# Performance work log

Measured on AMD Instinct MI355X. Metric: run time of the kernel, lower is better.

Reference implementation:

```python
import jax, jax.numpy as jnp
import numpy as np

# ---- config (matches init_kwargs) ----
L_LEVELS = 10          # int(log(8192/16)/log(2)) + 1
LEVEL_DIM = 4
BASE_RES = 16
LOG2_T = 21
BOUND = 2.0            # contract() output bound
DENSITY_BIAS = -1.0
RGB_PADDING = 0.001
DEG_VIEW = 4
PRIME1 = np.uint32(2654435761)
PRIME2 = np.uint32(805459861)


def _grid_meta():
    # torch-ngp GridEncoder layout: per-level scale = base*2^l - 1 (per_level_scale=2),
    # resolution = base*2^l, params = min(2^21, (res+1)^3) rounded up to multiple of 8.
    offsets, scales, res_list, sizes = [0], [], [], []
    for l in range(L_LEVELS):
        res = BASE_RES * (2 ** l)
        scales.append(float(res - 1))
        n = min(2 ** LOG2_T, (res + 1) ** 3)
        n = int(np.ceil(n / 8) * 8)
        res_list.append(res)
        sizes.append(n)
        offsets.append(offsets[-1] + n)
    return scales, res_list, sizes, offsets

GRID_SCALES, GRID_RES, GRID_SIZES, GRID_OFFSETS = _grid_meta()
TOTAL_PARAMS = GRID_OFFSETS[-1]  # 14995560
CORNERS = np.array([[(c >> d) & 1 for d in range(3)] for c in range(8)], dtype=np.int32)


def contract(x):
    # mipnerf360 contraction, output in [-2, 2]
    eps = jnp.finfo(x.dtype).eps
    x_mag_sq = jnp.maximum(eps, jnp.sum(x * x, axis=-1, keepdims=True))
    return jnp.where(x_mag_sq <= 1.0, x, ((2.0 * jnp.sqrt(x_mag_sq) - 1.0) / x_mag_sq) * x)


def pos_enc(x):
    # coord.pos_enc with identity, min_deg=0, max_deg=DEG_VIEW -> dim 3 + 3*2*4 = 27
    scales = 2.0 ** jnp.arange(DEG_VIEW, dtype=x.dtype)
    xb = (x[..., None, :] * scales[:, None]).reshape(x.shape[:-1] + (3 * DEG_VIEW,))
    four = jnp.sin(jnp.concatenate([xb, xb + 0.5 * jnp.pi], axis=-1))
    return jnp.concatenate([x, four], axis=-1)


def grid_encode(x01, embeddings):
    # x01: [N,3] in [0,1]; embeddings: [TOTAL_PARAMS, LEVEL_DIM]
    feats = []
    for l in range(L_LEVELS):
        pos = x01 * GRID_SCALES[l] + 0.5  # align_corners=False
        pos_floor = jnp.floor(pos)
        frac = pos - pos_floor            # trilinear weights, differentiable in x01
        pg = pos_floor.astype(jnp.int32)  # [N,3]
        res1 = GRID_RES[l] + 1
        size = GRID_SIZES[l]
        use_hash = (res1 ** 3) > size
        lvl_emb = embeddings[GRID_OFFSETS[l]:GRID_OFFSETS[l] + size]
        acc = jnp.zeros(x01.shape[:-1] + (LEVEL_DIM,), x01.dtype)
        for c in range(8):
            off = CORNERS[c]
            corner = pg + off[None, :]
            if use_hash:
                cu = corner.astype(jnp.uint32)
                idx = (cu[:, 0] ^ (cu[:, 1] * PRIME1) ^ (cu[:, 2] * PRIME2)) % jnp.uint32(size)
                idx = idx.astype(jnp.int32)
            else:
                idx = corner[:, 0] + corner[:, 1] * res1 + corner[:, 2] * (res1 * res1)
            w = jnp.prod(jnp.where(off[None, :] == 1, frac, 1.0 - frac), axis=-1)  # [N]
            acc = acc + w[:, None] * lvl_emb[idx]
        feats.append(acc)
    return jnp.concatenate(feats, axis=-1)  # [N, 40]


def setup_inputs() -> dict:
    key = jax.random.key(0)
    ks = jax.random.split(key, 10)
    R, S = 2048, 32
    coords = jax.random.normal(ks[0], (R, S, 3), jnp.float32) * 1.5
    viewdirs = jax.random.normal(ks[1], (R, 3), jnp.float32)
    viewdirs = viewdirs / jnp.linalg.norm(viewdirs, axis=-1, keepdims=True)
    embeddings = (jax.random.uniform(ks[2], (TOTAL_PARAMS, LEVEL_DIM), jnp.float32) * 2.0 - 1.0) * 1e-4

    def lin(k, fan_in, fan_out):
        k1, k2 = jax.random.split(k)
        lim = 1.0 / np.sqrt(fan_in)
        w = jax.random.uniform(k1, (fan_in, fan_out), jnp.float32, -lim, lim)
        b = jax.random.uniform(k2, (fan_out,), jnp.float32, -lim, lim)
        return w, b

    w_d1, b_d1 = lin(ks[3], L_LEVELS * LEVEL_DIM, 64)
    w_d2, b_d2 = lin(ks[4], 64, 256)
    DIR_DIM = 3 + 3 * 2 * DEG_VIEW  # 27
    w_r0, b_r0 = lin(ks[5], 256 + DIR_DIM, 256)          # 283 -> 256
    w_r1, b_r1 = lin(ks[6], 256 + 256 + DIR_DIM, 256)    # skip concat: 539 -> 256
    w_rgb, b_rgb = lin(ks[7], 256, 3)
    return dict(coords=coords, viewdirs=viewdirs, embeddings=embeddings,
                w_d1=w_d1, b_d1=b_d1, w_d2=w_d2, b_d2=b_d2,
                w_r0=w_r0, b_r0=b_r0, w_r1=w_r1, b_r1=b_r1,
                w_rgb=w_rgb, b_rgb=b_rgb)


def reference(coords, viewdirs, embeddings, w_d1, b_d1, w_d2, b_d2,
              w_r0, b_r0, w_r1, b_r1, w_rgb, b_rgb):
    shape = coords.shape[:-1]  # (rays, samples)
    cw = contract(coords) / BOUND          # coords_warped, in [-1, 1]
    x01 = (cw.reshape(-1, 3) + BOUND) / (2.0 * BOUND)  # encoder normalization with bound=2
    feats = grid_encode(x01, embeddings)               # [N, 40]
    h = jax.nn.relu(feats @ w_d1 + b_d1)
    x = h @ w_d2 + b_d2                                # [N, 256]
    raw_density = x[:, 0].reshape(shape)
    density = jax.nn.softplus(raw_density + DENSITY_BIAS)
    bottleneck = x.reshape(shape + (256,))
    dir_enc = pos_enc(viewdirs)                        # [rays, 27]
    dir_enc = jnp.broadcast_to(dir_enc[..., None, :], shape + (dir_enc.shape[-1],))
    inp = jnp.concatenate([bottleneck, dir_enc], axis=-1)  # [rays, S, 283]
    y = jax.nn.relu(inp @ w_r0 + b_r0)
    y = jnp.concatenate([y, inp], axis=-1)             # skip at layer i == skip_layer_dir == 0
    y = jax.nn.relu(y @ w_r1 + b_r1)
    rgb = jax.nn.sigmoid(y @ w_rgb + b_rgb)            # rgb_premultiplier=1, rgb_bias=0
    rgb = rgb * (1.0 + 2.0 * RGB_PADDING) - RGB_PADDING
    return cw, density, rgb
```

## Files before the change

### kernel.cpp

```cpp
#include <hip/hip_runtime.h>
#include <math.h>

#define NS 65536
#define NRAYS 2048

typedef __attribute__((ext_vector_type(8))) short short8;
typedef __attribute__((ext_vector_type(4))) float f32x4;
typedef unsigned short u16;

#define OFF_FEATS 0ull
#define OFF_HBF   10485760ull
#define OFF_DW0   85983232ull
#define OFF_DW1   88080384ull
#define OFF_WD2T  90177536ull
#define OFF_WR0T  90210304ull
#define OFF_WR1T  90341376ull

#define OUT_DENS 196608
#define OUT_RGB  262144

__device__ __forceinline__ u16 f2b(float f) {
    unsigned u = __builtin_bit_cast(unsigned, f);
    return (u16)((u + 0x7FFFu + ((u >> 16) & 1u)) >> 16);
}

__global__ __launch_bounds__(256) void cvt_weights(
    const float* __restrict__ w_d2, const float* __restrict__ w_r0,
    const float* __restrict__ w_r1, u16* __restrict__ wd2t,
    u16* __restrict__ wr0t, u16* __restrict__ wr1t)
{
    int idx = blockIdx.x * 256 + threadIdx.x;
    if (idx < 16384)  wd2t[idx] = f2b(w_d2[(idx & 63)  * 256 + (idx >> 6)]);
    if (idx < 65536)  wr0t[idx] = f2b(w_r0[(idx & 255) * 256 + (idx >> 8)]);
    if (idx < 131072) wr1t[idx] = f2b(w_r1[(idx & 511) * 256 + (idx >> 9)]);
}

__global__ __launch_bounds__(256) void dir_kernel(
    const float* __restrict__ viewdirs,
    const float* __restrict__ w_r0, const float* __restrict__ b_r0,
    const float* __restrict__ w_r1, const float* __restrict__ b_r1,
    float* __restrict__ dirW0, float* __restrict__ dirW1)
{
    __shared__ float de[27];
    int ray = blockIdx.x, t = threadIdx.x;
    if (t < 27) {
        float v;
        if (t < 3) v = viewdirs[3*ray + t];
        else {
            int k = (t - 3) % 12;
            float b = viewdirs[3*ray + (k % 3)] * (float)(1 << (k / 3));
            v = (t < 15) ? sinf(b) : sinf(b + 1.5707964f);
        }
        de[t] = v;
    }
    __syncthreads();
    float a0 = b_r0[t], a1 = b_r1[t];
#pragma unroll
    for (int d = 0; d < 27; ++d) {
        a0 = fmaf(de[d], w_r0[(256+d)*256 + t], a0);
        a1 = fmaf(de[d], w_r1[(512+d)*256 + t], a1);
    }
    dirW0[ray*256 + t] = a0;
    dirW1[ray*256 + t] = a1;
}

__global__ __launch_bounds__(256) void encode_kernel(
    const float* __restrict__ coords, const float* __restrict__ emb,
    float* __restrict__ cw_out, float* __restrict__ featsT)
{
    int t = threadIdx.x;
    int l = blockIdx.x >> 8;
    int i = ((blockIdx.x & 255) << 8) + t;
    float x = coords[3*i], y = coords[3*i+1], z = coords[3*i+2];
    float m2 = fmaxf(x*x + y*y + z*z, 1.1920928955078125e-07f);
    float cx = x, cy = y, cz = z;
    if (m2 > 1.0f) { float s = (2.0f*sqrtf(m2) - 1.0f)/m2; cx*=s; cy*=s; cz*=s; }
    cx *= 0.5f; cy *= 0.5f; cz *= 0.5f;
    if (l == 0) { cw_out[3*i]=cx; cw_out[3*i+1]=cy; cw_out[3*i+2]=cz; }
    float u0 = (cx + 2.0f)*0.25f, u1 = (cy + 2.0f)*0.25f, u2 = (cz + 2.0f)*0.25f;

    int res = 16 << l;
    int res1 = res + 1;
    float scale = (float)(res - 1);
    unsigned off = (l >= 3) ? 315496u + (unsigned)(l-3)*2097152u
                            : (l == 0 ? 0u : (l == 1 ? 4920u : 40864u));
    float p0 = u0*scale + 0.5f, p1 = u1*scale + 0.5f, p2 = u2*scale + 0.5f;
    float f0 = floorf(p0), f1 = floorf(p1), f2 = floorf(p2);
    float fr0 = p0-f0, fr1 = p1-f1, fr2 = p2-f2;
    unsigned g0 = (unsigned)(int)f0, g1 = (unsigned)(int)f1, g2 = (unsigned)(int)f2;
    float a0=0.f, a1=0.f, a2=0.f, a3=0.f;
    bool use_hash = (l >= 3);
#pragma unroll
    for (int c = 0; c < 8; ++c) {
        unsigned ox = c & 1u, oy = (c >> 1) & 1u, oz = (c >> 2) & 1u;
        unsigned qx = g0 + ox, qy = g1 + oy, qz = g2 + oz;
        unsigned idx;
        if (use_hash) idx = (qx ^ (qy*2654435761u) ^ (qz*805459861u)) & 2097151u;
        else          idx = qx + qy*(unsigned)res1 + qz*(unsigned)(res1*res1);
        const float4 e = *(const float4*)(emb + 4u*(off + idx));
        float w = (ox ? fr0 : 1.0f-fr0) * (oy ? fr1 : 1.0f-fr1) * (oz ? fr2 : 1.0f-fr2);
        a0 = fmaf(w, e.x, a0); a1 = fmaf(w, e.y, a1);
        a2 = fmaf(w, e.z, a2); a3 = fmaf(w, e.w, a3);
    }
    featsT[(4*l+0)*NS + i] = a0;
    featsT[(4*l+1)*NS + i] = a1;
    featsT[(4*l+2)*NS + i] = a2;
    featsT[(4*l+3)*NS + i] = a3;
}

__global__ __launch_bounds__(256) void gemm_d1_kernel(
    const float* __restrict__ featsT, const float* __restrict__ w_d1,
    const float* __restrict__ b_d1, const float* __restrict__ w_d2,
    const float* __restrict__ b_d2, u16* __restrict__ h_bf,
    float* __restrict__ dens)
{
    __shared__ float As[40][256];
    __shared__ float Ws[40*64];
    __shared__ float wc0[64];
    int t = threadIdx.x;
    int m0 = blockIdx.x * 256;
#pragma unroll
    for (int k = 0; k < 40; ++k) As[k][t] = featsT[k*NS + m0 + t];
#pragma unroll
    for (int i = 0; i < 10; ++i) Ws[i*256 + t] = w_d1[i*256 + t];
    if (t < 64) wc0[t] = w_d2[t*256];
    __syncthreads();
    int tn = t & 3, tm = t >> 2;
    float acc[4][16] = {};
#pragma unroll
    for (int k = 0; k < 40; ++k) {
        float4 a = *(const float4*)&As[k][tm*4];
        float av[4] = {a.x, a.y, a.z, a.w};
        const float4* wp = (const float4*)&Ws[k*64 + tn*16];
#pragma unroll
        for (int r = 0; r < 4; ++r) {
            float4 w = wp[r];
            float wv[4] = {w.x, w.y, w.z, w.w};
#pragma unroll
            for (int ii = 0; ii < 4; ++ii)
#pragma unroll
                for (int cc = 0; cc < 4; ++cc)
                    acc[ii][r*4+cc] = fmaf(av[ii], wv[cc], acc[ii][r*4+cc]);
        }
    }
    float p[4] = {0.f, 0.f, 0.f, 0.f};
#pragma unroll
    for (int jj = 0; jj < 16; ++jj) {
        int j = tn*16 + jj;
        float bj = b_d1[j], w0 = wc0[j];
#pragma unroll
        for (int ii = 0; ii < 4; ++ii) {
            float h = fmaxf(acc[ii][jj] + bj, 0.f);
            acc[ii][jj] = h;
            p[ii] = fmaf(h, w0, p[ii]);
        }
    }
#pragma unroll
    for (int ii = 0; ii < 4; ++ii) {
        int s = m0 + tm*4 + ii;
        unsigned u[8];
#pragma unroll
        for (int q = 0; q < 8; ++q)
            u[q] = (unsigned)f2b(acc[ii][2*q]) | ((unsigned)f2b(acc[ii][2*q+1]) << 16);
        uint4 v0 = {u[0], u[1], u[2], u[3]};
        uint4 v1 = {u[4], u[5], u[6], u[7]};
        *(uint4*)(h_bf + (size_t)s*64 + tn*16)     = v0;
        *(uint4*)(h_bf + (size_t)s*64 + tn*16 + 8) = v1;
    }
#pragma unroll
    for (int ii = 0; ii < 4; ++ii) {
        p[ii] += __shfl_xor(p[ii], 1, 64);
        p[ii] += __shfl_xor(p[ii], 2, 64);
    }
    if (tn == 0) {
        float b0 = b_d2[0];
#pragma unroll
        for (int ii = 0; ii < 4; ++ii) {
            float z = p[ii] + b0 - 1.0f;
            dens[m0 + tm*4 + ii] = fmaxf(z, 0.f) + log1pf(expf(-fabsf(z)));
        }
    }
}

#define MFMA __builtin_amdgcn_mfma_f32_16x16x32_bf16

__global__ __launch_bounds__(256) void mfma_tail(
    const u16* __restrict__ h_bf, const u16* __restrict__ wd2t,
    const u16* __restrict__ w0t, const u16* __restrict__ w1t,
    const float* __restrict__ b_d2, const float* __restrict__ dirW0,
    const float* __restrict__ dirW1, const float* __restrict__ w_rgb,
    const float* __restrict__ b_rgb, float* __restrict__ rgb)
{
    __shared__ u16 tileX[8192];
    __shared__ u16 tileY[8192];
    __shared__ float pp[4][32][3];
    int t = threadIdx.x, lane = t & 63, w = t >> 6;
    int m0 = blockIdx.x * 32;
    int rl = lane & 15, kg = (lane >> 4) * 8;
    int ro = (lane >> 4) * 4;
    unsigned swA = ((unsigned)(rl & 7)) << 4;
    const char* txc = (const char*)tileX;
    const char* tyc = (const char*)tileY;
    f32x4 zero = {0.f,0.f,0.f,0.f};

    f32x4 acc[2][4];

#pragma unroll
    for (int a = 0; a < 2; ++a)
#pragma unroll
        for (int b = 0; b < 4; ++b) acc[a][b] = zero;
    {
        const u16* pA0 = h_bf + (size_t)(m0 + rl)*64 + kg;
        const u16* pA1 = h_bf + (size_t)(m0 + 16 + rl)*64 + kg;
        const u16* pBd = wd2t + (w*64 + rl)*64 + kg;
#pragma unroll
        for (int ks = 0; ks < 2; ++ks) {
            int kb = ks*32;
            short8 a0 = *(const short8*)(pA0 + kb);
            short8 a1 = *(const short8*)(pA1 + kb);
#pragma unroll
            for (int nt = 0; nt < 4; ++nt) {
                short8 b = *(const short8*)(pBd + nt*1024 + kb);
                acc[0][nt] = MFMA(a0, b, acc[0][nt], 0, 0, 0);
                acc[1][nt] = MFMA(a1, b, acc[1][nt], 0, 0, 0);
            }
        }
    }
#pragma unroll
    for (int nt = 0; nt < 4; ++nt) {
        int col = w*64 + nt*16 + rl;
        float bias = b_d2[col];
#pragma unroll
        for (int mt = 0; mt < 2; ++mt)
#pragma unroll
            for (int r = 0; r < 4; ++r) {
                int row = mt*16 + ro + r;
                unsigned byte = (unsigned)(row*512 + col*2) ^ ((unsigned)(row & 7) << 4);
                tileX[byte >> 1] = f2b(acc[mt][nt][r] + bias);
            }
    }
    __syncthreads();

#pragma unroll
    for (int a = 0; a < 2; ++a)
#pragma unroll
        for (int b = 0; b < 4; ++b) acc[a][b] = zero;
    {
        const u16* pB0 = w0t + (w*64 + rl)*256 + kg;
#pragma unroll
        for (int ks = 0; ks < 8; ++ks) {
            int kb = ks*32;
            unsigned base = (unsigned)((kb + kg)*2);
            short8 a0 = *(const short8*)(txc + (((unsigned)(rl*512)      + base) ^ swA));
            short8 a1 = *(const short8*)(txc + (((unsigned)((16+rl)*512) + base) ^ swA));
#pragma unroll
            for (int nt = 0; nt < 4; ++nt) {
                short8 b = *(const short8*)(pB0 + nt*4096 + kb);
                acc[0][nt] = MFMA(a0, b, acc[0][nt], 0, 0, 0);
                acc[1][nt] = MFMA(a1, b, acc[1][nt], 0, 0, 0);
            }
        }
    }
    {
        const float* dir0 = dirW0 + (m0 >> 5)*256;
#pragma unroll
        for (int nt = 0; nt < 4; ++nt) {
            int col = w*64 + nt*16 + rl;
            float bias = dir0[col];
#pragma unroll
            for (int mt = 0; mt < 2; ++mt)
#pragma unroll
                for (int r = 0; r < 4; ++r) {
                    int row = mt*16 + ro + r;
                    unsigned byte = (unsigned)(row*512 + col*2) ^ ((unsigned)(row & 7) << 4);
                    tileY[byte >> 1] = f2b(fmaxf(acc[mt][nt][r] + bias, 0.f));
                }
        }
    }
    __syncthreads();

#pragma unroll
    for (int a = 0; a < 2; ++a)
#pragma unroll
        for (int b = 0; b < 4; ++b) acc[a][b] = zero;
    {
        const u16* pB1 = w1t + (w*64 + rl)*512 + kg;
#pragma unroll
        for (int ks = 0; ks < 8; ++ks) {
            int kb = 256 + ks*32;
            unsigned base = (unsigned)((ks*32 + kg)*2);
            short8 a0 = *(const short8*)(txc + (((unsigned)(rl*512)      + base) ^ swA));
            short8 a1 = *(const short8*)(txc + (((unsigned)((16+rl)*512) + base) ^ swA));
#pragma unroll
            for (int nt = 0; nt < 4; ++nt) {
                short8 b = *(const short8*)(pB1 + nt*8192 + kb);
                acc[0][nt] = MFMA(a0, b, acc[0][nt], 0, 0, 0);
                acc[1][nt] = MFMA(a1, b, acc[1][nt], 0, 0, 0);
            }
        }
#pragma unroll
        for (int ks = 0; ks < 8; ++ks) {
            int kb = ks*32;
            unsigned base = (unsigned)((kb + kg)*2);
            short8 a0 = *(const short8*)(tyc + (((unsigned)(rl*512)      + base) ^ swA));
            short8 a1 = *(const short8*)(tyc + (((unsigned)((16+rl)*512) + base) ^ swA));
#pragma unroll
            for (int nt = 0; nt < 4; ++nt) {
                short8 b = *(const short8*)(pB1 + nt*8192 + kb);
                acc[0][nt] = MFMA(a0, b, acc[0][nt], 0, 0, 0);
                acc[1][nt] = MFMA(a1, b, acc[1][nt], 0, 0, 0);
            }
        }
    }

    {
        const float* dir1 = dirW1 + (m0 >> 5)*256;
        float p[2][4][3];
#pragma unroll
        for (int mt = 0; mt < 2; ++mt)
#pragma unroll
            for (int r = 0; r < 4; ++r)
                p[mt][r][0] = p[mt][r][1] = p[mt][r][2] = 0.f;
#pragma unroll
        for (int nt = 0; nt < 4; ++nt) {
            int col = w*64 + nt*16 + rl;
            float dv = dir1[col];
            float w0 = w_rgb[col*3], w1 = w_rgb[col*3+1], w2 = w_rgb[col*3+2];
#pragma unroll
            for (int mt = 0; mt < 2; ++mt)
#pragma unroll
                for (int r = 0; r < 4; ++r) {
                    float y1 = fmaxf(acc[mt][nt][r] + dv, 0.f);
                    p[mt][r][0] = fmaf(y1, w0, p[mt][r][0]);
                    p[mt][r][1] = fmaf(y1, w1, p[mt][r][1]);
                    p[mt][r][2] = fmaf(y1, w2, p[mt][r][2]);
                }
        }
#pragma unroll
        for (int mask = 1; mask < 16; mask <<= 1)
#pragma unroll
            for (int mt = 0; mt < 2; ++mt)
#pragma unroll
                for (int r = 0; r < 4; ++r)
#pragma unroll
                    for (int c = 0; c < 3; ++c)
                        p[mt][r][c] += __shfl_xor(p[mt][r][c], mask, 64);
        if (rl == 0) {
#pragma unroll
            for (int mt = 0; mt < 2; ++mt)
#pragma unroll
                for (int r = 0; r < 4; ++r) {
                    int row = mt*16 + ro + r;
                    pp[w][row][0] = p[mt][r][0];
                    pp[w][row][1] = p[mt][r][1];
                    pp[w][row][2] = p[mt][r][2];
                }
        }
    }
    __syncthreads();
    if (t < 96) {
        int row = t / 3, c = t - row*3;
        float v = pp[0][row][c] + pp[1][row][c] + pp[2][row][c] + pp[3][row][c]
                + b_rgb[c];
        float sg = 1.0f / (1.0f + expf(-v));
        rgb[(m0 + row)*3 + c] = sg * 1.002f - 0.001f;
    }
}

extern "C" void kernel_launch(void* const* d_in, const int* in_sizes, int n_in,
                              void* d_out, int out_size, void* d_ws, size_t ws_size,
                              hipStream_t stream)
{
    const float* coords   = (const float*)d_in[0];
    const float* viewdirs = (const float*)d_in[1];
    const float* emb      = (const float*)d_in[2];
    const float* w_d1     = (const float*)d_in[3];
    const float* b_d1     = (const float*)d_in[4];
    const float* w_d2     = (const float*)d_in[5];
    const float* b_d2     = (const float*)d_in[6];
    const float* w_r0     = (const float*)d_in[7];
    const float* b_r0     = (const float*)d_in[8];
    const float* w_r1     = (const float*)d_in[9];
    const float* b_r1     = (const float*)d_in[10];
    const float* w_rgb    = (const float*)d_in[11];
    const float* b_rgb    = (const float*)d_in[12];

    float* out  = (float*)d_out;
    float* cw   = out;
    float* dens = out + OUT_DENS;
    float* rgb  = out + OUT_RGB;

    char* wsB = (char*)d_ws;
    float* featsT = (float*)(wsB + OFF_FEATS);
    u16*   h_bf   = (u16*)(wsB + OFF_HBF);
    float* dirW0  = (float*)(wsB + OFF_DW0);
    float* dirW1  = (float*)(wsB + OFF_DW1);
    u16*   wd2t   = (u16*)(wsB + OFF_WD2T);
    u16*   wr0t   = (u16*)(wsB + OFF_WR0T);
    u16*   wr1t   = (u16*)(wsB + OFF_WR1T);

    cvt_weights<<<512, 256, 0, stream>>>(w_d2, w_r0, w_r1, wd2t, wr0t, wr1t);
    dir_kernel<<<NRAYS, 256, 0, stream>>>(viewdirs, w_r0, b_r0, w_r1, b_r1, dirW0, dirW1);
    encode_kernel<<<2560, 256, 0, stream>>>(coords, emb, cw, featsT);
    gemm_d1_kernel<<<NS/256, 256, 0, stream>>>(featsT, w_d1, b_d1, w_d2, b_d2, h_bf, dens);
    mfma_tail<<<NS/32, 256, 0, stream>>>(h_bf, wd2t, wr0t, wr1t, b_d2,
                                         dirW0, dirW1, w_rgb, b_rgb, rgb);
}
```

Baseline: 462.2 us.

## Merge encode, dir and weight-convert kernels into one launch; shrink d1 GEMM tiles

Three independent preprocessing kernels (hash-grid encode, view-direction projection, weight bf16 transpose) become one kernel with block-index dispatch, removing two launches and their serialization gaps. The first dense-layer GEMM now uses 64-sample blocks with one sample per thread instead of four, giving 1024 blocks rather than 256 for better occupancy across CUs. In exchange each thread does less register-level reuse of the weights, and the fused kernel mixes very different block types.

```diff
diff --git a/kernel.cpp b/kernel.cpp
--- a/kernel.cpp
+++ b/kernel.cpp
@@ -24,88 +24,83 @@
     return (u16)((u + 0x7FFFu + ((u >> 16) & 1u)) >> 16);
 }
 
-__global__ __launch_bounds__(256) void cvt_weights(
+__global__ __launch_bounds__(256) void fused_pre(
+    const float* __restrict__ coords, const float* __restrict__ emb,
+    const float* __restrict__ viewdirs,
     const float* __restrict__ w_d2, const float* __restrict__ w_r0,
-    const float* __restrict__ w_r1, u16* __restrict__ wd2t,
-    u16* __restrict__ wr0t, u16* __restrict__ wr1t)
+    const float* __restrict__ b_r0, const float* __restrict__ w_r1,
+    const float* __restrict__ b_r1,
+    float* __restrict__ cw_out, float* __restrict__ featsT,
+    float* __restrict__ dirW0, float* __restrict__ dirW1,
+    u16* __restrict__ wd2t, u16* __restrict__ wr0t, u16* __restrict__ wr1t)
 {
-    int idx = blockIdx.x * 256 + threadIdx.x;
-    if (idx < 16384)  wd2t[idx] = f2b(w_d2[(idx & 63)  * 256 + (idx >> 6)]);
-    if (idx < 65536)  wr0t[idx] = f2b(w_r0[(idx & 255) * 256 + (idx >> 8)]);
-    if (idx < 131072) wr1t[idx] = f2b(w_r1[(idx & 511) * 256 + (idx >> 9)]);
-}
-
-__global__ __launch_bounds__(256) void dir_kernel(
-    const float* __restrict__ viewdirs,
-    const float* __restrict__ w_r0, const float* __restrict__ b_r0,
-    const float* __restrict__ w_r1, const float* __restrict__ b_r1,
-    float* __restrict__ dirW0, float* __restrict__ dirW1)
-{
-    __shared__ float de[27];
-    int ray = blockIdx.x, t = threadIdx.x;
-    if (t < 27) {
-        float v;
-        if (t < 3) v = viewdirs[3*ray + t];
-        else {
-            int k = (t - 3) % 12;
-            float b = viewdirs[3*ray + (k % 3)] * (float)(1 << (k / 3));
-            v = (t < 15) ? sinf(b) : sinf(b + 1.5707964f);
-        }
-        de[t] = v;
-    }
-    __syncthreads();
-    float a0 = b_r0[t], a1 = b_r1[t];
-#pragma unroll
-    for (int d = 0; d < 27; ++d) {
-        a0 = fmaf(de[d], w_r0[(256+d)*256 + t], a0);
-        a1 = fmaf(de[d], w_r1[(512+d)*256 + t], a1);
-    }
-    dirW0[ray*256 + t] = a0;
-    dirW1[ray*256 + t] = a1;
-}
-
-__global__ __launch_bounds__(256) void encode_kernel(
-    const float* __restrict__ coords, const float* __restrict__ emb,
-    float* __restrict__ cw_out, float* __restrict__ featsT)
-{
-    int t = threadIdx.x;
-    int l = blockIdx.x >> 8;
-    int i = ((blockIdx.x & 255) << 8) + t;
-    float x = coords[3*i], y = coords[3*i+1], z = coords[3*i+2];
-    float m2 = fmaxf(x*x + y*y + z*z, 1.1920928955078125e-07f);
-    float cx = x, cy = y, cz = z;
-    if (m2 > 1.0f) { float s = (2.0f*sqrtf(m2) - 1.0f)/m2; cx*=s; cy*=s; cz*=s; }
-    cx *= 0.5f; cy *= 0.5f; cz *= 0.5f;
-    if (l == 0) { cw_out[3*i]=cx; cw_out[3*i+1]=cy; cw_out[3*i+2]=cz; }
-    float u0 = (cx + 2.0f)*0.25f, u1 = (cy + 2.0f)*0.25f, u2 = (cz + 2.0f)*0.25f;
-
-    int res = 16 << l;
-    int res1 = res + 1;
-    float scale = (float)(res - 1);
-    unsigned off = (l >= 3) ? 315496u + (unsigned)(l-3)*2097152u
-                            : (l == 0 ? 0u : (l == 1 ? 4920u : 40864u));
-    float p0 = u0*scale + 0.5f, p1 = u1*scale + 0.5f, p2 = u2*scale + 0.5f;
-    float f0 = floorf(p0), f1 = floorf(p1), f2 = floorf(p2);
-    float fr0 = p0-f0, fr1 = p1-f1, fr2 = p2-f2;
-    unsigned g0 = (unsigned)(int)f0, g1 = (unsigned)(int)f1, g2 = (unsigned)(int)f2;
-    float a0=0.f, a1=0.f, a2=0.f, a3=0.f;
-    bool use_hash = (l >= 3);
-#pragma unroll
-    for (int c = 0; c < 8; ++c) {
-        unsigned ox = c & 1u, oy = (c >> 1) & 1u, oz = (c >> 2) & 1u;
-        unsigned qx = g0 + ox, qy = g1 + oy, qz = g2 + oz;
-        unsigned idx;
-        if (use_hash) idx = (qx ^ (qy*2654435761u) ^ (qz*805459861u)) & 2097151u;
-        else          idx = qx + qy*(unsigned)res1 + qz*(unsigned)(res1*res1);
-        const float4 e = *(const float4*)(emb + 4u*(off + idx));
-        float w = (ox ? fr0 : 1.0f-fr0) * (oy ? fr1 : 1.0f-fr1) * (oz ? fr2 : 1.0f-fr2);
-        a0 = fmaf(w, e.x, a0); a1 = fmaf(w, e.y, a1);
-        a2 = fmaf(w, e.z, a2); a3 = fmaf(w, e.w, a3);
-    }
-    featsT[(4*l+0)*NS + i] = a0;
-    featsT[(4*l+1)*NS + i] = a1;
-    featsT[(4*l+2)*NS + i] = a2;
-    featsT[(4*l+3)*NS + i] = a3;
+    int b = blockIdx.x, t = threadIdx.x;
+    if (b < 2560) {
+        int l = b >> 8;
+        int i = ((b & 255) << 8) + t;
+        float x = coords[3*i], y = coords[3*i+1], z = coords[3*i+2];
+        float m2 = fmaxf(x*x + y*y + z*z, 1.1920928955078125e-07f);
+        float cx = x, cy = y, cz = z;
+        if (m2 > 1.0f) { float s = (2.0f*sqrtf(m2) - 1.0f)/m2; cx*=s; cy*=s; cz*=s; }
+        cx *= 0.5f; cy *= 0.5f; cz *= 0.5f;
+        if (l == 0) { cw_out[3*i]=cx; cw_out[3*i+1]=cy; cw_out[3*i+2]=cz; }
+        float u0 = (cx + 2.0f)*0.25f, u1 = (cy + 2.0f)*0.25f, u2 = (cz + 2.0f)*0.25f;
+
+        int res = 16 << l;
+        int res1 = res + 1;
+        float scale = (float)(res - 1);
+        unsigned off = (l >= 3) ? 315496u + (unsigned)(l-3)*2097152u
+                                : (l == 0 ? 0u : (l == 1 ? 4920u : 40864u));
+        float p0 = u0*scale + 0.5f, p1 = u1*scale + 0.5f, p2 = u2*scale + 0.5f;
+        float f0 = floorf(p0), f1 = floorf(p1), f2 = floorf(p2);
+        float fr0 = p0-f0, fr1 = p1-f1, fr2 = p2-f2;
+        unsigned g0 = (unsigned)(int)f0, g1 = (unsigned)(int)f1, g2 = (unsigned)(int)f2;
+        float a0=0.f, a1=0.f, a2=0.f, a3=0.f;
+        bool use_hash = (l >= 3);
+#pragma unroll
+        for (int c = 0; c < 8; ++c) {
+            unsigned ox = c & 1u, oy = (c >> 1) & 1u, oz = (c >> 2) & 1u;
+            unsigned qx = g0 + ox, qy = g1 + oy, qz = g2 + oz;
+            unsigned idx;
+            if (use_hash) idx = (qx ^ (qy*2654435761u) ^ (qz*805459861u)) & 2097151u;
+            else          idx = qx + qy*(unsigned)res1 + qz*(unsigned)(res1*res1);
+            const float4 e = *(const float4*)(emb + 4u*(off + idx));
+            float w = (ox ? fr0 : 1.0f-fr0) * (oy ? fr1 : 1.0f-fr1) * (oz ? fr2 : 1.0f-fr2);
+            a0 = fmaf(w, e.x, a0); a1 = fmaf(w, e.y, a1);
+            a2 = fmaf(w, e.z, a2); a3 = fmaf(w, e.w, a3);
+        }
+        featsT[(4*l+0)*NS + i] = a0;
+        featsT[(4*l+1)*NS + i] = a1;
+        featsT[(4*l+2)*NS + i] = a2;
+        featsT[(4*l+3)*NS + i] = a3;
+    } else if (b < 4608) {
+        __shared__ float de[27];
+        int ray = b - 2560;
+        if (t < 27) {
+            float v;
+            if (t < 3) v = viewdirs[3*ray + t];
+            else {
+                int k = (t - 3) % 12;
+                float bb = viewdirs[3*ray + (k % 3)] * (float)(1 << (k / 3));
+                v = (t < 15) ? sinf(bb) : sinf(bb + 1.5707964f);
+            }
+            de[t] = v;
+        }
+        __syncthreads();
+        float a0 = b_r0[t], a1 = b_r1[t];
+#pragma unroll
+        for (int d = 0; d < 27; ++d) {
+            a0 = fmaf(de[d], w_r0[(256+d)*256 + t], a0);
+            a1 = fmaf(de[d], w_r1[(512+d)*256 + t], a1);
+        }
+        dirW0[ray*256 + t] = a0;
+        dirW1[ray*256 + t] = a1;
+    } else {
+        int idx = (b - 4608) * 256 + t;
+        if (idx < 16384)  wd2t[idx] = f2b(w_d2[(idx & 63)  * 256 + (idx >> 6)]);
+        if (idx < 65536)  wr0t[idx] = f2b(w_r0[(idx & 255) * 256 + (idx >> 8)]);
+        if (idx < 131072) wr1t[idx] = f2b(w_r1[(idx & 511) * 256 + (idx >> 9)]);
+    }
 }
 
 __global__ __launch_bounds__(256) void gemm_d1_kernel(
@@ -114,71 +109,60 @@
     const float* __restrict__ b_d2, u16* __restrict__ h_bf,
     float* __restrict__ dens)
 {
-    __shared__ float As[40][256];
+    __shared__ float As[40][64];
     __shared__ float Ws[40*64];
     __shared__ float wc0[64];
     int t = threadIdx.x;
-    int m0 = blockIdx.x * 256;
-#pragma unroll
-    for (int k = 0; k < 40; ++k) As[k][t] = featsT[k*NS + m0 + t];
-#pragma unroll
-    for (int i = 0; i < 10; ++i) Ws[i*256 + t] = w_d1[i*256 + t];
+    int m0 = blockIdx.x * 64;
+#pragma unroll
+    for (int i = 0; i < 10; ++i) {
+        int idx = i*256 + t;
+        int k = idx >> 6, s = idx & 63;
+        As[k][s] = featsT[k*NS + m0 + s];
+        Ws[idx]  = w_d1[idx];
+    }
     if (t < 64) wc0[t] = w_d2[t*256];
     __syncthreads();
-    int tn = t & 3, tm = t >> 2;
-    float acc[4][16] = {};
+    int cg = t & 3, sm = t >> 2;
+    float acc[16] = {};
 #pragma unroll
     for (int k = 0; k < 40; ++k) {
-        float4 a = *(const float4*)&As[k][tm*4];
-        float av[4] = {a.x, a.y, a.z, a.w};
-        const float4* wp = (const float4*)&Ws[k*64 + tn*16];
-#pragma unroll
-        for (int r = 0; r < 4; ++r) {
-            float4 w = wp[r];
-            float wv[4] = {w.x, w.y, w.z, w.w};
-#pragma unroll
-            for (int ii = 0; ii < 4; ++ii)
-#pragma unroll
-                for (int cc = 0; cc < 4; ++cc)
-                    acc[ii][r*4+cc] = fmaf(av[ii], wv[cc], acc[ii][r*4+cc]);
-        }
-    }
-    float p[4] = {0.f, 0.f, 0.f, 0.f};
+        float a = As[k][sm];
+        const float4* wp = (const float4*)&Ws[k*64 + cg*16];
+#pragma unroll
+        for (int q = 0; q < 4; ++q) {
+            float4 w = wp[q];
+            acc[q*4+0] = fmaf(a, w.x, acc[q*4+0]);
+            acc[q*4+1] = fmaf(a, w.y, acc[q*4+1]);
+            acc[q*4+2] = fmaf(a, w.z, acc[q*4+2]);
+            acc[q*4+3] = fmaf(a, w.w, acc[q*4+3]);
+        }
+    }
+    float p = 0.f;
+    float hv[16];
 #pragma unroll
     for (int jj = 0; jj < 16; ++jj) {
-        int j = tn*16 + jj;
-        float bj = b_d1[j], w0 = wc0[j];
-#pragma unroll
-        for (int ii = 0; ii < 4; ++ii) {
-            float h = fmaxf(acc[ii][jj] + bj, 0.f);
-            acc[ii][jj] = h;
-            p[ii] = fmaf(h, w0, p[ii]);
-        }
-    }
-#pragma unroll
-    for (int ii = 0; ii < 4; ++ii) {
-        int s = m0 + tm*4 + ii;
+        int j = cg*16 + jj;
+        float h = fmaxf(acc[jj] + b_d1[j], 0.f);
+        hv[jj] = h;
+        p = fmaf(h, wc0[j], p);
+    }
+    {
+        int s = m0 + sm;
         unsigned u[8];
 #pragma unroll
         for (int q = 0; q < 8; ++q)
-            u[q] = (unsigned)f2b(acc[ii][2*q]) | ((unsigned)f2b(acc[ii][2*q+1]) << 16);
+            u[q] = (unsigned)f2b(hv[2*q]) | ((unsigned)f2b(hv[2*q+1]) << 16);
         uint4 v0 = {u[0], u[1], u[2], u[3]};
         uint4 v1 = {u[4], u[5], u[6], u[7]};
-        *(uint4*)(h_bf + (size_t)s*64 + tn*16)     = v0;
-        *(uint4*)(h_bf + (size_t)s*64 + tn*16 + 8) = v1;
-    }
-#pragma unroll
-    for (int ii = 0; ii < 4; ++ii) {
-        p[ii] += __shfl_xor(p[ii], 1, 64);
-        p[ii] += __shfl_xor(p[ii], 2, 64);
-    }
-    if (tn == 0) {
-        float b0 = b_d2[0];
-#pragma unroll
-        for (int ii = 0; ii < 4; ++ii) {
-            float z = p[ii] + b0 - 1.0f;
-            dens[m0 + tm*4 + ii] = fmaxf(z, 0.f) + log1pf(expf(-fabsf(z)));
-        }
+        *(uint4*)(h_bf + (size_t)s*64 + cg*16)     = v0;
+        *(uint4*)(h_bf + (size_t)s*64 + cg*16 + 8) = v1;
+    }
+    p += __shfl_xor(p, 1, 64);
+    p += __shfl_xor(p, 2, 64);
+    if (cg == 0) {
+        float z = p + b_d2[0] - 1.0f;
+        dens[m0 + sm] = fmaxf(z, 0.f) + log1pf(expf(-fabsf(z)));
     }
 }
 
@@ -399,10 +383,10 @@
     u16*   wr0t   = (u16*)(wsB + OFF_WR0T);
     u16*   wr1t   = (u16*)(wsB + OFF_WR1T);
 
-    cvt_weights<<<512, 256, 0, stream>>>(w_d2, w_r0, w_r1, wd2t, wr0t, wr1t);
-    dir_kernel<<<NRAYS, 256, 0, stream>>>(viewdirs, w_r0, b_r0, w_r1, b_r1, dirW0, dirW1);
-    encode_kernel<<<2560, 256, 0, stream>>>(coords, emb, cw, featsT);
-    gemm_d1_kernel<<<NS/256, 256, 0, stream>>>(featsT, w_d1, b_d1, w_d2, b_d2, h_bf, dens);
+    fused_pre<<<5120, 256, 0, stream>>>(coords, emb, viewdirs, w_d2, w_r0, b_r0,
+                                        w_r1, b_r1, cw, featsT, dirW0, dirW1,
+                                        wd2t, wr0t, wr1t);
+    gemm_d1_kernel<<<NS/64, 256, 0, stream>>>(featsT, w_d1, b_d1, w_d2, b_d2, h_bf, dens);
     mfma_tail<<<NS/32, 256, 0, stream>>>(h_bf, wd2t, wr0t, wr1t, b_d2,
                                          dirW0, dirW1, w_rgb, b_rgb, rgb);
 }
```

Measured after the change: 454.1 us. Within noise of the previous version (-1.7%).
